# Kernel optimization log

Measured on AMD Instinct MI355X. Metric: run time of the kernel, lower is better.

The kernel has to match this reference:

```python
import jax, jax.numpy as jnp
import numpy as np

# dims (Nemotron-H 8B class mamba mixer)
HID = 4096      # hidden_size
NH = 128        # mamba_num_heads
HD = 64         # mamba_head_dim
DIN = NH * HD   # intermediate_size = 8192
G = 8           # n_groups
N = 128         # ssm_state_size
K = 4           # conv_kernel
CS = 256        # chunk_size
EPS = 1e-5
GROUP_SIZE = DIN // G
CONV_DIM = DIN + 2 * G * N           # 10240
PROJ = DIN + CONV_DIM + NH           # 18560 = gate | xBC | dt


def segment_sum(x):
    """x: [..., k] -> [..., k, k]; out[i,j] = sum_{m=j+1..i} x[m], -inf above diag."""
    k = x.shape[-1]
    xe = jnp.broadcast_to(x[..., None], x.shape + (k,))
    xe = jnp.where(jnp.tril(jnp.ones((k, k), bool), -1), xe, 0.0)
    s = jnp.cumsum(xe, axis=-2)
    return jnp.where(jnp.tril(jnp.ones((k, k), bool), 0), s, -jnp.inf)


def setup_inputs() -> dict:
    key = jax.random.key(0)
    ks = jax.random.split(key, 9)
    std = 0.02
    return {
        "hidden_states": jax.random.normal(ks[0], (2, 2048, HID), jnp.float32),
        "in_proj_w": jax.random.normal(ks[1], (PROJ, HID), jnp.float32) * std,
        "conv_w": jax.random.normal(ks[2], (CONV_DIM, 1, K), jnp.float32) * 0.1,
        "conv_b": jax.random.normal(ks[3], (CONV_DIM,), jnp.float32) * 0.01,
        "dt_bias": jax.random.uniform(ks[4], (NH,), jnp.float32, -4.0, -2.0),
        "A_log": jnp.log(jax.random.uniform(ks[5], (NH,), jnp.float32, 1.0, 16.0)),
        "D": jnp.ones((NH,), jnp.float32),
        "norm_w": jnp.ones((DIN,), jnp.float32),
        "out_proj_w": jax.random.normal(ks[8], (HID, DIN), jnp.float32) * std,
    }


def reference(hidden_states, in_proj_w, conv_w, conv_b, dt_bias, A_log, D, norm_w, out_proj_w):
    b, l, _ = hidden_states.shape
    zxbcdt = hidden_states @ in_proj_w.T                       # [b,l,PROJ]
    gate = zxbcdt[..., :DIN]
    xBC = zxbcdt[..., DIN:DIN + CONV_DIM]
    dt = zxbcdt[..., DIN + CONV_DIM:]                          # [b,l,NH]

    # causal depthwise conv1d + silu
    conv = jax.lax.conv_general_dilated(
        jnp.transpose(xBC, (0, 2, 1)), conv_w, (1,), [(K - 1, 0)],
        feature_group_count=CONV_DIM, dimension_numbers=("NCH", "OIH", "NCH"))
    xBC = jax.nn.silu(jnp.transpose(conv + conv_b[None, :, None], (0, 2, 1)))

    x = xBC[..., :DIN].reshape(b, l, NH, HD)
    B = xBC[..., DIN:DIN + G * N].reshape(b, l, G, N)
    C = xBC[..., DIN + G * N:].reshape(b, l, G, N)
    B = jnp.repeat(B, NH // G, axis=2)                         # [b,l,NH,N]
    C = jnp.repeat(C, NH // G, axis=2)

    A = -jnp.exp(A_log)                                        # [NH]
    dt = jax.nn.softplus(dt + dt_bias)                         # [b,l,NH]; limit (0,inf) is a no-op

    pad = (CS - l % CS) % CS
    def padl(t):
        return jnp.pad(t, [(0, 0), (0, pad)] + [(0, 0)] * (t.ndim - 2))

    D_res = D[None, None, :, None] * padl(x)                   # [b,L,NH,HD]
    xs = x * dt[..., None]
    Adt = A[None, None, :] * dt                                # [b,l,NH]

    nc = (l + pad) // CS
    def chunk(t):
        return padl(t).reshape((b, nc, CS) + t.shape[2:])
    xs, B, C = chunk(xs), chunk(B), chunk(C)                   # [b,c,k,h,*]
    Ac = jnp.transpose(chunk(Adt), (0, 3, 1, 2))               # [b,h,c,k]
    A_cumsum = jnp.cumsum(Ac, axis=-1)

    # 1. intra-chunk (diagonal blocks)
    L = jnp.exp(segment_sum(Ac))                               # [b,h,c,k,k]
    Gm = jnp.einsum("bcihn,bcjhn->bhcij", C, B)
    Y_diag = jnp.einsum("bhcij,bcjhd->bcihd", Gm * L, xs)

    # 2. chunk states
    decay_states = jnp.exp(A_cumsum[..., -1:] - A_cumsum)      # [b,h,c,k]
    states = jnp.einsum("bckhn,bhck,bckhd->bchdn", B, decay_states, xs)

    # 3. inter-chunk recurrence
    A_tail = jnp.pad(A_cumsum[..., -1], ((0, 0), (0, 0), (1, 0)))
    decay_chunk = jnp.exp(segment_sum(A_tail))                 # [b,h,c+1,c+1]
    states = jnp.concatenate([jnp.zeros_like(states[:, :1]), states], axis=1)
    new_states = jnp.einsum("bhzc,bchdn->bzhdn", decay_chunk, states)
    states = new_states[:, :-1]                                # [b,c,h,d,n]

    # 4. state -> output
    state_decay = jnp.exp(A_cumsum)                            # [b,h,c,k]
    Y_off = jnp.einsum("bckhn,bchdn,bhck->bckhd", C, states, state_decay)

    y = (Y_diag + Y_off).reshape(b, l + pad, NH, HD) + D_res
    y = y[:, :l].reshape(b, l, DIN)

    # gated grouped RMSNorm
    y = y * jax.nn.silu(gate)
    yg = y.reshape(b, l, G, GROUP_SIZE)
    var = jnp.mean(yg * yg, axis=-1, keepdims=True)
    y = (yg * jax.lax.rsqrt(var + EPS)).reshape(b, l, DIN) * norm_w
    return y @ out_proj_w.T
```

## Files before the change

### kernel.cpp

```cpp
#include <hip/hip_runtime.h>
#include <hip/hip_bf16.h>
#include <math.h>

#define HID 4096
#define NH 128
#define HD 64
#define DIN 8192
#define G 8
#define NSTATE 128
#define CS 256
#define GROUP_SIZE 1024
#define CONV_DIM 10240
#define ZXW 18432
#define BATCH 2
#define SEQ 2048
#define NT (BATCH*SEQ)
#define NC 8
#define DTSK 16

typedef __attribute__((ext_vector_type(8))) short bf16x8;
typedef __attribute__((ext_vector_type(4))) float f32x4;
typedef __attribute__((ext_vector_type(8))) unsigned short u16x8;
typedef __attribute__((ext_vector_type(4))) unsigned short u16x4;

__device__ __forceinline__ float sigmoidf_(float x){ return 1.f/(1.f+expf(-x)); }
__device__ __forceinline__ float siluf_(float x){ return x*sigmoidf_(x); }
__device__ __forceinline__ float softplusf_(float x){ return (x>20.f)? x : log1pf(expf(x)); }
__device__ __forceinline__ float b2f(unsigned short u){ union{unsigned int i; float f;} x; x.i = ((unsigned int)u)<<16; return x.f; }
__device__ __forceinline__ unsigned short f2b(float f){ __hip_bfloat16 h = __float2bfloat16(f); return *(unsigned short*)&h; }

__device__ __forceinline__ void gload_lds16(const void* g, void* l) {
  __builtin_amdgcn_global_load_lds((const __attribute__((address_space(1))) unsigned int*)g,
                                   (__attribute__((address_space(3))) unsigned int*)l, 16, 0, 0);
}
__device__ __forceinline__ bf16x8 ld8bf(const __hip_bfloat16* p){ return *(const bf16x8*)p; }

__device__ __forceinline__ void cast8(const float* in, __hip_bfloat16* out) {
  const float4* p = (const float4*)in;
  float4 a = p[0], b = p[1];
  union { __hip_bfloat16 h[8]; int4 v; } o;
  o.h[0]=__float2bfloat16(a.x); o.h[1]=__float2bfloat16(a.y);
  o.h[2]=__float2bfloat16(a.z); o.h[3]=__float2bfloat16(a.w);
  o.h[4]=__float2bfloat16(b.x); o.h[5]=__float2bfloat16(b.y);
  o.h[6]=__float2bfloat16(b.z); o.h[7]=__float2bfloat16(b.w);
  *(int4*)out = o.v;
}

__global__ __launch_bounds__(256)
void cast2_kernel(const float* __restrict__ w_in, __hip_bfloat16* __restrict__ w_in_bf,
                  const float* __restrict__ w_out, __hip_bfloat16* __restrict__ w_out_bf) {
  const size_t n1 = (size_t)ZXW*HID/8;
  const size_t n2 = (size_t)HID*DIN/8;
  const size_t ntot = n1 + n2;
  size_t i = (size_t)blockIdx.x * 256 + threadIdx.x;
  size_t stride = (size_t)gridDim.x * 256;
  for (; i < ntot; i += stride) {
    if (i < n1)  cast8(w_in + i*8,      w_in_bf + i*8);
    else         cast8(w_out+ (i-n1)*8, w_out_bf+ (i-n1)*8);
  }
}

template<bool OUT_BF16>
__global__ __launch_bounds__(512)
void gemm_bf16_256(const __hip_bfloat16* __restrict__ A, const __hip_bfloat16* __restrict__ B,
                   void* __restrict__ Cout, int M, int N, int K) {
  const int nMt = M >> 8, nNt = N >> 8;
  const int nwg = nMt * nNt;
  const int cpx = nwg >> 3;
  const int lin = blockIdx.x;
  const int swz = (lin & 7) * cpx + (lin >> 3);
  const int mt = swz % nMt, ntile = swz / nMt;
  const int rowBase = mt << 8;
  const int colBase = ntile << 8;

  __shared__ short As[4][8192];
  __shared__ short Bs[4][8192];

  const int tid = threadIdx.x;
  const int lane = tid & 63, wid = tid >> 6;
  const int wr = wid >> 2, wc = wid & 3;
  const int l15 = lane & 15, l4 = lane >> 4;

  const int r0 = tid >> 2,        c0 = (tid & 3) ^ ((r0 >> 1) & 3);
  const int r1 = (512+tid) >> 2,  c1 = ((512+tid) & 3) ^ ((r1 >> 1) & 3);
  const __hip_bfloat16* gA0 = A + (size_t)(rowBase + r0)*K + c0*8;
  const __hip_bfloat16* gA1 = A + (size_t)(rowBase + r1)*K + c1*8;
  const __hip_bfloat16* gB0 = B + (size_t)(colBase + r0)*K + c0*8;
  const __hip_bfloat16* gB1 = B + (size_t)(colBase + r1)*K + c1*8;
  const int ld0 = wid*512, ld1 = 4096 + wid*512;

#define STAGE_A(q, kt) do { \
    gload_lds16(gA0 + (size_t)(kt)*32, (void*)&As[q][ld0]); \
    gload_lds16(gA1 + (size_t)(kt)*32, (void*)&As[q][ld1]); \
  } while(0)
#define STAGE_B(q, kt) do { \
    gload_lds16(gB0 + (size_t)(kt)*32, (void*)&Bs[q][ld0]); \
    gload_lds16(gB1 + (size_t)(kt)*32, (void*)&Bs[q][ld1]); \
  } while(0)

  int aoff[8], boff[4];
  #pragma unroll
  for (int m=0;m<8;++m){ int r = wr*128 + m*16 + l15; aoff[m] = r*32 + ((l4 ^ ((r>>1)&3))*8); }
  #pragma unroll
  for (int n=0;n<4;++n){ int r = wc*64  + n*16 + l15; boff[n] = r*32 + ((l4 ^ ((r>>1)&3))*8); }

  f32x4 acc[8][4] = {};
  const int NKT = K >> 5;

  STAGE_A(0,0); STAGE_B(0,0);
  STAGE_A(1,1); STAGE_B(1,1);
  STAGE_A(2,2); STAGE_B(2,2);
  asm volatile("s_waitcnt vmcnt(8)" ::: "memory");
  __builtin_amdgcn_s_barrier();

  for (int t = 0; t < NKT; ++t) {
    const short* ab = &As[t&3][0];
    const short* bb = &Bs[t&3][0];
    const int q3 = (t+3)&3;
    bf16x8 a[4], b[4], a2[4];
    #pragma unroll
    for (int m=0;m<4;++m) a[m] = *(const bf16x8*)&ab[aoff[m]];
    #pragma unroll
    for (int n=0;n<4;++n) b[n] = *(const bf16x8*)&bb[boff[n]];
    if (t + 3 < NKT) STAGE_A(q3, t+3);
    __builtin_amdgcn_s_barrier();
    asm volatile("s_waitcnt lgkmcnt(0)" ::: "memory");
    __builtin_amdgcn_sched_barrier(0);
    __builtin_amdgcn_s_setprio(1);
    #pragma unroll
    for (int m=0;m<4;++m)
      #pragma unroll
      for (int n=0;n<4;++n)
        acc[m][n] = __builtin_amdgcn_mfma_f32_16x16x32_bf16(a[m], b[n], acc[m][n], 0, 0, 0);
    __builtin_amdgcn_s_setprio(0);
    __builtin_amdgcn_s_barrier();
    #pragma unroll
    for (int m=0;m<4;++m) a2[m] = *(const bf16x8*)&ab[aoff[m+4]];
    if (t + 3 < NKT) STAGE_B(q3, t+3);
    const int rem = NKT - 1 - t;
    if (rem >= 3)      asm volatile("s_waitcnt vmcnt(8)" ::: "memory");
    else if (rem == 2) asm volatile("s_waitcnt vmcnt(4)" ::: "memory");
    else if (rem == 1) asm volatile("s_waitcnt vmcnt(0)" ::: "memory");
    __builtin_amdgcn_s_barrier();
    asm volatile("s_waitcnt lgkmcnt(0)" ::: "memory");
    __builtin_amdgcn_sched_barrier(0);
    __builtin_amdgcn_s_setprio(1);
    #pragma unroll
    for (int m=0;m<4;++m)
      #pragma unroll
      for (int n=0;n<4;++n)
        acc[m+4][n] = __builtin_amdgcn_mfma_f32_16x16x32_bf16(a2[m], b[n], acc[m+4][n], 0, 0, 0);
    __builtin_amdgcn_s_setprio(0);
    __builtin_amdgcn_s_barrier();
  }
#undef STAGE_A
#undef STAGE_B

  #pragma unroll
  for (int m=0;m<8;++m) {
    int row0 = rowBase + wr*128 + m*16 + l4*4;
    #pragma unroll
    for (int n=0;n<4;++n) {
      int col = colBase + wc*64 + n*16 + l15;
      #pragma unroll
      for (int j=0;j<4;++j) {
        if (OUT_BF16)
          ((__hip_bfloat16*)Cout)[(size_t)(row0+j)*N + col] = __float2bfloat16(acc[m][n][j]);
        else
          ((float*)Cout)[(size_t)(row0+j)*N + col] = acc[m][n][j];
      }
    }
  }
}

__global__ __launch_bounds__(256)
void dt_gemm_splitk(const float* __restrict__ A, const float* __restrict__ B,
                    float* __restrict__ partial, __hip_bfloat16* __restrict__ hs_bf) {
  __shared__ float As[16][132];
  __shared__ float Bs[16][132];
  const int tid = threadIdx.x;
  const int tx = tid & 15, ty = tid >> 4;
  const int rowBase = blockIdx.y * 128;
  const int k0 = blockIdx.x * (HID/DTSK);
  float acc[8][8] = {};
  for (int kt = k0; kt < k0 + HID/DTSK; kt += 16) {
    for (int e = tid; e < 128*16; e += 256) {
      int r = e >> 4, c = e & 15;
      float av = A[(size_t)(rowBase + r) * HID + kt + c];
      As[c][r] = av;
      hs_bf[(size_t)(rowBase + r) * HID + kt + c] = __float2bfloat16(av);
      Bs[c][r] = B[(size_t)r * HID + kt + c];
    }
    __syncthreads();
    #pragma unroll
    for (int kk = 0; kk < 16; ++kk) {
      float a[8], bv[8];
      #pragma unroll
      for (int i = 0; i < 8; ++i) a[i] = As[kk][ty*8+i];
      #pragma unroll
      for (int j = 0; j < 8; ++j) bv[j] = Bs[kk][tx*8+j];
      #pragma unroll
      for (int i = 0; i < 8; ++i)
        #pragma unroll
        for (int j = 0; j < 8; ++j)
          acc[i][j] += a[i]*bv[j];
    }
    __syncthreads();
  }
  float* outp = partial + (size_t)blockIdx.x * NT * NH;
  for (int i = 0; i < 8; ++i) {
    size_t ro = (size_t)(rowBase + ty*8 + i) * NH + tx*8;
    #pragma unroll
    for (int j = 0; j < 8; ++j) outp[ro + j] = acc[i][j];
  }
}

__global__ __launch_bounds__(256)
void dt_scan_kernel(const float* __restrict__ partial, const float* __restrict__ dt_bias,
                    const float* __restrict__ A_log, float* __restrict__ dt_sp,
                    float* __restrict__ Acs) {
  int bid = blockIdx.x;
  int c = bid % NC;
  int h = (bid / NC) % NH;
  int b = bid / (NC*NH);
  int k = threadIdx.x;
  int t = b*SEQ + c*CS + k;
  float raw = dt_bias[h];
  #pragma unroll
  for (int sk = 0; sk < DTSK; ++sk) raw += partial[(size_t)sk*NT*NH + (size_t)t*NH + h];
  float dtv = softplusf_(raw);
  dt_sp[(size_t)t*NH + h] = dtv;
  float adt = -expf(A_log[h]) * dtv;
  __shared__ float s[CS];
  s[k] = adt;
  __syncthreads();
  for (int off = 1; off < CS; off <<= 1) {
    float v = (k >= off) ? s[k-off] : 0.f;
    __syncthreads();
    s[k] += v;
    __syncthreads();
  }
  Acs[((size_t)(b*NH + h)*NC + c)*CS + k] = s[k];
}

__global__ __launch_bounds__(256)
void conv_fused_kernel(const __hip_bfloat16* __restrict__ zx, const float* __restrict__ w,
                       const float* __restrict__ bias,
                       const float* __restrict__ dt_sp, const float* __restrict__ Acs,
                       __hip_bfloat16* __restrict__ xsT, __hip_bfloat16* __restrict__ xwT,
                       __hip_bfloat16* __restrict__ Bbf, __hip_bfloat16* __restrict__ Cbf,
                       __hip_bfloat16* __restrict__ BT) {
  const int tt = blockIdx.x;
  const int ct = blockIdx.y;
  const int t0 = tt*64;
  const int ch0 = ct*64;
  const int tid = threadIdx.x;
  __shared__ unsigned short T[64][72];
  __shared__ float dts[64], ews[64];

  const bool isX = (ch0 < DIN);
  const bool isB = (ch0 >= DIN) && (ch0 < DIN + G*NSTATE);

  if (isX && tid < 64) {
    int h = ch0 >> 6;
    int t = t0 + tid;
    dts[tid] = dt_sp[(size_t)t*NH + h];
    int b = t0 >> 11, cc = (t0 >> 8) & 7, k0 = t0 & 255;
    const float* acs = Acs + ((size_t)(b*NH+h)*NC + cc)*CS;
    ews[tid] = __expf(acs[CS-1] - acs[k0 + tid]);
  }

  const int l0 = t0 & (SEQ-1);
  #pragma unroll
  for (int it = 0; it < 2; ++it) {
    int r = tid >> 2;
    int c8 = (tid & 3) + it*4;
    int cb = ch0 + c8*8;
    float acc[8];
    *(float4*)&acc[0] = *(const float4*)&bias[cb];
    *(float4*)&acc[4] = *(const float4*)&bias[cb+4];
    float4 wv[8];
    #pragma unroll
    for (int q=0;q<8;++q) wv[q] = *(const float4*)&w[(cb+q)*4];
    #pragma unroll
    for (int k=0;k<4;++k) {
      if (l0 + r - 3 + k >= 0) {
        u16x8 v = *(const u16x8*)&zx[(size_t)(t0+r-3+k)*ZXW + DIN + cb];
        #pragma unroll
        for (int q=0;q<8;++q) acc[q] += b2f(v[q]) * ((const float*)&wv[q])[k];
      }
    }
    u16x8 o;
    #pragma unroll
    for (int q=0;q<8;++q) o[q] = f2b(siluf_(acc[q]));
    if (isX || isB) {
      #pragma unroll
      for (int q=0;q<8;++q) T[c8*8+q][r] = o[q];
    }
    if (!isX) {
      if (isB) *(u16x8*)&Bbf[(size_t)(t0+r)*(G*NSTATE) + (cb - DIN)] = o;
      else     *(u16x8*)&Cbf[(size_t)(t0+r)*(G*NSTATE) + (cb - DIN - G*NSTATE)] = o;
    }
  }
  if (!isX && !isB) return;
  __syncthreads();
  #pragma unroll
  for (int it = 0; it < 2; ++it) {
    int ch = tid >> 2;
    int tc = (tid & 3) + it*4;
    u16x8 v = *(const u16x8*)&T[ch][tc*8];
    if (isX) {
      u16x8 a, wv2;
      #pragma unroll
      for (int q=0;q<8;++q) {
        float f = b2f(v[q]);
        float fs = f * dts[tc*8+q];
        a[q]   = f2b(fs);
        wv2[q] = f2b(fs * ews[tc*8+q]);
      }
      *(u16x8*)&xsT[(size_t)(ch0+ch)*NT + t0 + tc*8] = a;
      *(u16x8*)&xwT[(size_t)(ch0+ch)*NT + t0 + tc*8] = wv2;
    } else {
      *(u16x8*)&BT[(size_t)(ch0 - DIN + ch)*NT + t0 + tc*8] = v;
    }
  }
}

__global__ __launch_bounds__(256)
void chunk_states_fused(const __hip_bfloat16* __restrict__ xwT, const __hip_bfloat16* __restrict__ BT,
                        const float* __restrict__ Acs, __hip_bfloat16* __restrict__ states_bf) {
  int h = blockIdx.x, b = blockIdx.y;
  int g = h >> 4;
  int tid = threadIdx.x, lane = tid & 63, w = tid >> 6;
  int l15 = lane & 15, l4 = lane >> 4;
  int n0 = w*32;
  f32x4 S[4][2] = {};
  for (int c = 0; c < NC; ++c) {
    int tbase = b*SEQ + c*CS;
    const __hip_bfloat16* xp = xwT + (size_t)(h*64 + l15)*NT + tbase + l4*8;
    const __hip_bfloat16* bp = BT + (size_t)(g*128 + n0 + l15)*NT + tbase + l4*8;
    f32x4 acc[4][2] = {};
    for (int kc = 0; kc < 8; ++kc) {
      bf16x8 xf[4], bf2[2];
      #pragma unroll
      for (int tm=0;tm<4;++tm) xf[tm] = ld8bf(xp + (size_t)(tm*16)*NT + kc*32);
      #pragma unroll
      for (int tn=0;tn<2;++tn) bf2[tn] = ld8bf(bp + (size_t)(tn*16)*NT + kc*32);
      #pragma unroll
      for (int tm=0;tm<4;++tm)
        #pragma unroll
        for (int tn=0;tn<2;++tn)
          acc[tm][tn] = __builtin_amdgcn_mfma_f32_16x16x32_bf16(xf[tm], bf2[tn], acc[tm][tn], 0, 0, 0);
    }
    __hip_bfloat16* out = states_bf + ((size_t)(b*NC + c)*NH + h)*(HD*NSTATE);
    float decay = expf(Acs[((size_t)(b*NH+h)*NC + c)*CS + CS-1]);
    #pragma unroll
    for (int tm=0;tm<4;++tm)
      #pragma unroll
      for (int tn=0;tn<2;++tn)
        #pragma unroll
        for (int q=0;q<4;++q) {
          out[(size_t)(tm*16 + l4*4 + q)*NSTATE + n0 + tn*16 + l15] = __float2bfloat16(S[tm][tn][q]);
          S[tm][tn][q] = S[tm][tn][q]*decay + acc[tm][tn][q];
        }
  }
}

__global__ __launch_bounds__(256)
void y_mfma_kernel(const __hip_bfloat16* __restrict__ zx,
                   const __hip_bfloat16* __restrict__ Cn,
                   const __hip_bfloat16* __restrict__ Bn,
                   const __hip_bfloat16* __restrict__ xsT,
                   const __hip_bfloat16* __restrict__ Sbf,
                   const float* __restrict__ dt_sp,
                   const float* __restrict__ Acs,
                   const float* __restrict__ Dp,
                   __hip_bfloat16* __restrict__ ybf) {
  int h = blockIdx.x;
  int bc = blockIdx.y;
  int c = bc & 7, b = bc >> 3;
  int g = h >> 4;
  int tbase = b*SEQ + c*CS;
  int tid = threadIdx.x, lane = tid & 63, w = tid >> 6;
  int l15 = lane & 15, l4 = lane >> 4;
  int i0 = w*64;
  __shared__ float acs_s[CS];
  __shared__ unsigned short P[4][64][72];
  acs_s[tid] = Acs[((size_t)(b*NH+h)*NC + c)*CS + tid];
  __syncthreads();

  float acs_i[4], rd[4];
  float Dh = Dp[h];
  #pragma unroll
  for (int ti=0;ti<4;++ti) {
    int ig = i0 + ti*16 + l15;
    acs_i[ti] = acs_s[ig];
    rd[ti] = Dh / dt_sp[(size_t)(tbase+ig)*NH + h];
  }
  const __hip_bfloat16* Cbase = Cn + (size_t)tbase*1024 + g*128;
  const __hip_bfloat16* Bbase = Bn + (size_t)tbase*1024 + g*128;
  const __hip_bfloat16* xbase = xsT + (size_t)(h*64 + l15)*NT + tbase;

  f32x4 accY[4][4] = {};
  for (int jb = 0; jb <= w; ++jb) {
    int j0 = jb*64;
    f32x4 sacc[4][4] = {};
    for (int kc = 0; kc < 4; ++kc) {
      bf16x8 bfr[4], cfr[4];
      #pragma unroll
      for (int tj=0;tj<4;++tj) bfr[tj] = ld8bf(Bbase + (size_t)(j0 + tj*16 + l15)*1024 + kc*32 + l4*8);
      #pragma unroll
      for (int ti=0;ti<4;++ti) cfr[ti] = ld8bf(Cbase + (size_t)(i0 + ti*16 + l15)*1024 + kc*32 + l4*8);
      #pragma unroll
      for (int tj=0;tj<4;++tj)
        #pragma unroll
        for (int ti=0;ti<4;++ti)
          sacc[tj][ti] = __builtin_amdgcn_mfma_f32_16x16x32_bf16(bfr[tj], cfr[ti], sacc[tj][ti], 0, 0, 0);
    }
    #pragma unroll
    for (int tj=0;tj<4;++tj)
      #pragma unroll
      for (int ti=0;ti<4;++ti) {
        int ig = i0 + ti*16 + l15;
        float ai = acs_i[ti];
        u16x4 pk;
        #pragma unroll
        for (int q=0;q<4;++q) {
          int jg = j0 + tj*16 + l4*4 + q;
          float v = (jg <= ig) ? sacc[tj][ti][q] * __expf(ai - acs_s[jg]) : 0.f;
          if (jg == ig) v += rd[ti];
          pk[q] = f2b(v);
        }
        *(u16x4*)&P[w][ti*16 + l15][tj*16 + l4*4] = pk;
      }
    #pragma unroll
    for (int kc2 = 0; kc2 < 2; ++kc2) {
      bf16x8 xf[4], pf[4];
      #pragma unroll
      for (int tm=0;tm<4;++tm) xf[tm] = ld8bf(xbase + (size_t)(tm*16)*NT + j0 + kc2*32 + l4*8);
      #pragma unroll
      for (int ti=0;ti<4;++ti) pf[ti] = *(const bf16x8*)&P[w][ti*16 + l15][kc2*32 + l4*8];
      #pragma unroll
      for (int tm=0;tm<4;++tm)
        #pragma unroll
        for (int ti=0;ti<4;++ti)
          accY[tm][ti] = __builtin_amdgcn_mfma_f32_16x16x32_bf16(xf[tm], pf[ti], accY[tm][ti], 0, 0, 0);
    }
  }
  const __hip_bfloat16* Sb = Sbf + ((size_t)bc*NH + h)*(HD*NSTATE);
  f32x4 oacc[4][4] = {};
  for (int kc = 0; kc < 4; ++kc) {
    bf16x8 sf[4], cfr[4];
    #pragma unroll
    for (int tm=0;tm<4;++tm) sf[tm] = ld8bf(Sb + (size_t)(tm*16 + l15)*NSTATE + kc*32 + l4*8);
    #pragma unroll
    for (int ti=0;ti<4;++ti) cfr[ti] = ld8bf(Cbase + (size_t)(i0 + ti*16 + l15)*1024 + kc*32 + l4*8);
    #pragma unroll
    for (int tm=0;tm<4;++tm)
      #pragma unroll
      for (int ti=0;ti<4;++ti)
        oacc[tm][ti] = __builtin_amdgcn_mfma_f32_16x16x32_bf16(sf[tm], cfr[ti], oacc[tm][ti], 0, 0, 0);
  }
  #pragma unroll
  for (int ti=0;ti<4;++ti) {
    int ig = i0 + ti*16 + l15;
    int t = tbase + ig;
    float sd = __expf(acs_i[ti]);
    #pragma unroll
    for (int tm=0;tm<4;++tm) {
      int ch0 = h*64 + tm*16 + l4*4;
      u16x4 gv = *(const u16x4*)&zx[(size_t)t*ZXW + ch0];
      u16x4 out;
      #pragma unroll
      for (int q=0;q<4;++q) {
        float yv = accY[tm][ti][q] + sd * oacc[tm][ti][q];
        yv *= siluf_(b2f(gv[q]));
        out[q] = f2b(yv);
      }
      *(u16x4*)&ybf[(size_t)t*DIN + ch0] = out;
    }
  }
}

__global__ __launch_bounds__(256)
void groupnorm_bf16_kernel(unsigned short* __restrict__ y, const float* __restrict__ norm_w) {
  int bid = blockIdx.x;
  int g = bid % G;
  int t = bid / G;
  unsigned short* yp = y + (size_t)t*DIN + g*GROUP_SIZE;
  int tid = threadIdx.x;
  u16x4 v = *(const u16x4*)&yp[tid*4];
  float f[4]; float ss = 0.f;
  #pragma unroll
  for (int j=0;j<4;++j) { f[j] = b2f(v[j]); ss += f[j]*f[j]; }
  #pragma unroll
  for (int off = 32; off > 0; off >>= 1) ss += __shfl_xor(ss, off);
  __shared__ float wsum[4];
  int wave = tid >> 6;
  if ((tid & 63) == 0) wsum[wave] = ss;
  __syncthreads();
  float tot = wsum[0]+wsum[1]+wsum[2]+wsum[3];
  float rs = rsqrtf(tot/(float)GROUP_SIZE + 1e-5f);
  const float* nw = norm_w + g*GROUP_SIZE + tid*4;
  u16x4 o;
  #pragma unroll
  for (int j=0;j<4;++j) o[j] = f2b(f[j] * rs * nw[j]);
  *(u16x4*)&yp[tid*4] = o;
}

extern "C" void kernel_launch(void* const* d_in, const int* in_sizes, int n_in,
                              void* d_out, int out_size, void* d_ws, size_t ws_size,
                              hipStream_t stream) {
  const float* hs        = (const float*)d_in[0];
  const float* in_proj_w = (const float*)d_in[1];
  const float* conv_w    = (const float*)d_in[2];
  const float* conv_b    = (const float*)d_in[3];
  const float* dt_bias   = (const float*)d_in[4];
  const float* A_log     = (const float*)d_in[5];
  const float* Dp        = (const float*)d_in[6];
  const float* norm_w    = (const float*)d_in[7];
  const float* out_proj_w= (const float*)d_in[8];
  float* outp = (float*)d_out;

  char* ws = (char*)d_ws;
  __hip_bfloat16* zx_bf = (__hip_bfloat16*)ws;
  char* p = ws + (size_t)NT*ZXW*2;
  __hip_bfloat16* B_bf  = (__hip_bfloat16*)p; p += (size_t)NT*G*NSTATE*2;
  __hip_bfloat16* C_bf  = (__hip_bfloat16*)p; p += (size_t)NT*G*NSTATE*2;
  __hip_bfloat16* BT    = (__hip_bfloat16*)p; p += (size_t)NT*G*NSTATE*2;
  __hip_bfloat16* y_bf  = (__hip_bfloat16*)p; p += (size_t)NT*DIN*2;
  float* dtb    = (float*)p;  p += (size_t)NT*NH*4;
  float* Acs    = (float*)p;  p += (size_t)BATCH*NH*NC*CS*4;
  float* dt_part = (float*)y_bf;
  char* F = p;
  __hip_bfloat16* w_in_bf   = (__hip_bfloat16*)F;
  __hip_bfloat16* xsT       = (__hip_bfloat16*)F;
  __hip_bfloat16* xwT       = (__hip_bfloat16*)(F + 67108864);
  __hip_bfloat16* hs_bf     = (__hip_bfloat16*)(F + 150994944);
  __hip_bfloat16* states_bf = (__hip_bfloat16*)(F + 150994944);
  char* F2 = F + 150994944 + 33554432;
  __hip_bfloat16* w_out_bf  = (__hip_bfloat16*)F2;

  dt_gemm_splitk<<<dim3(DTSK, NT/128), 256, 0, stream>>>(hs, in_proj_w + (size_t)ZXW*HID, dt_part, hs_bf);
  dt_scan_kernel<<<BATCH*NH*NC, CS, 0, stream>>>(dt_part, dt_bias, A_log, dtb, Acs);

  cast2_kernel<<<4096, 256, 0, stream>>>(in_proj_w, w_in_bf, out_proj_w, w_out_bf);

  gemm_bf16_256<true><<<dim3((NT/256)*(ZXW/256)), 512, 0, stream>>>(
      hs_bf, w_in_bf, zx_bf, NT, ZXW, HID);

  conv_fused_kernel<<<dim3(NT/64, CONV_DIM/64), 256, 0, stream>>>(
      zx_bf, conv_w, conv_b, dtb, Acs, xsT, xwT, B_bf, C_bf, BT);

  chunk_states_fused<<<dim3(NH, BATCH), 256, 0, stream>>>(xwT, BT, Acs, states_bf);

  y_mfma_kernel<<<dim3(NH, BATCH*NC), 256, 0, stream>>>(zx_bf, C_bf, B_bf, xsT, states_bf, dtb, Acs, Dp, y_bf);
  groupnorm_bf16_kernel<<<NT*G, 256, 0, stream>>>((unsigned short*)y_bf, norm_w);

  gemm_bf16_256<false><<<dim3((NT/256)*(HID/256)), 512, 0, stream>>>(
      y_bf, w_out_bf, outp, NT, HID, DIN);
}
```

Measured before the change: 1.798 ms.

## Restructure bf16 GEMM mainloop into 8-phase ping-pong pipeline with K=64 tiles

```diff
diff --git a/kernel.cpp b/kernel.cpp
--- a/kernel.cpp
+++ b/kernel.cpp
@@ -61,7 +61,7 @@
 }
 
 template<bool OUT_BF16>
-__global__ __launch_bounds__(512)
+__global__ __launch_bounds__(512, 2)
 void gemm_bf16_256(const __hip_bfloat16* __restrict__ A, const __hip_bfloat16* __restrict__ B,
                    void* __restrict__ Cout, int M, int N, int K) {
   const int nMt = M >> 8, nNt = N >> 8;
@@ -73,88 +73,105 @@
   const int rowBase = mt << 8;
   const int colBase = ntile << 8;
 
-  __shared__ short As[4][8192];
-  __shared__ short Bs[4][8192];
+  __shared__ short As[2][2][8192];
+  __shared__ short Bs[2][2][8192];
 
   const int tid = threadIdx.x;
   const int lane = tid & 63, wid = tid >> 6;
   const int wr = wid >> 2, wc = wid & 3;
   const int l15 = lane & 15, l4 = lane >> 4;
 
-  const int r0 = tid >> 2,        c0 = (tid & 3) ^ ((r0 >> 1) & 3);
-  const int r1 = (512+tid) >> 2,  c1 = ((512+tid) & 3) ^ ((r1 >> 1) & 3);
-  const __hip_bfloat16* gA0 = A + (size_t)(rowBase + r0)*K + c0*8;
-  const __hip_bfloat16* gA1 = A + (size_t)(rowBase + r1)*K + c1*8;
-  const __hip_bfloat16* gB0 = B + (size_t)(colBase + r0)*K + c0*8;
-  const __hip_bfloat16* gB1 = B + (size_t)(colBase + r1)*K + c1*8;
-  const int ld0 = wid*512, ld1 = 4096 + wid*512;
-
-#define STAGE_A(q, kt) do { \
-    gload_lds16(gA0 + (size_t)(kt)*32, (void*)&As[q][ld0]); \
-    gload_lds16(gA1 + (size_t)(kt)*32, (void*)&As[q][ld1]); \
+  const int r0 = tid >> 2;
+  const int c0 = (tid & 3) ^ ((r0 >> 1) & 3);
+  const __hip_bfloat16* gA = A + (size_t)(rowBase + r0)*K + c0*8;
+  const __hip_bfloat16* gB = B + (size_t)(colBase + r0)*K + c0*8;
+  const int wdst = wid * 512;
+
+#define STG(Ld, gp, h, kt) do { \
+    gload_lds16(gp + (size_t)((h)*128)*K + (size_t)(kt)*64,      (void*)&(Ld)[wdst]); \
+    gload_lds16(gp + (size_t)((h)*128)*K + (size_t)(kt)*64 + 32, (void*)&(Ld)[4096 + wdst]); \
   } while(0)
-#define STAGE_B(q, kt) do { \
-    gload_lds16(gB0 + (size_t)(kt)*32, (void*)&Bs[q][ld0]); \
-    gload_lds16(gB1 + (size_t)(kt)*32, (void*)&Bs[q][ld1]); \
+
+  const int xg = (l4 ^ ((l15 >> 1) & 3)) * 8;
+  int aofs[8], bofs[4];
+  #pragma unroll
+  for (int m=0;m<8;++m) aofs[m] = (m*16 + l15)*32 + xg;
+  #pragma unroll
+  for (int n=0;n<4;++n) bofs[n] = ((wc&1)*64 + n*16 + l15)*32 + xg;
+
+  bf16x8 Af[4][2], Bf[4][2];
+  f32x4 acc[8][4] = {};
+
+#define RDA(bb, mh) do { \
+    const short* s_ = &As[bb][wr][0]; \
+    _Pragma("unroll") for (int m=0;m<4;++m) { \
+      Af[m][0] = *(const bf16x8*)&s_[aofs[(mh)*4+m]]; \
+      Af[m][1] = *(const bf16x8*)&s_[4096 + aofs[(mh)*4+m]]; } \
   } while(0)
-
-  int aoff[8], boff[4];
-  #pragma unroll
-  for (int m=0;m<8;++m){ int r = wr*128 + m*16 + l15; aoff[m] = r*32 + ((l4 ^ ((r>>1)&3))*8); }
-  #pragma unroll
-  for (int n=0;n<4;++n){ int r = wc*64  + n*16 + l15; boff[n] = r*32 + ((l4 ^ ((r>>1)&3))*8); }
-
-  f32x4 acc[8][4] = {};
-  const int NKT = K >> 5;
-
-  STAGE_A(0,0); STAGE_B(0,0);
-  STAGE_A(1,1); STAGE_B(1,1);
-  STAGE_A(2,2); STAGE_B(2,2);
-  asm volatile("s_waitcnt vmcnt(8)" ::: "memory");
+#define RDB(bb, nh) do { \
+    const short* s_ = &Bs[bb][wc>>1][0]; \
+    _Pragma("unroll") for (int n=0;n<2;++n) { \
+      Bf[(nh)*2+n][0] = *(const bf16x8*)&s_[bofs[(nh)*2+n]]; \
+      Bf[(nh)*2+n][1] = *(const bf16x8*)&s_[4096 + bofs[(nh)*2+n]]; } \
+  } while(0)
+#define MFQ(mh, nh) do { \
+    __builtin_amdgcn_s_setprio(1); \
+    _Pragma("unroll") for (int m=0;m<4;++m) \
+      _Pragma("unroll") for (int n=0;n<2;++n) \
+        _Pragma("unroll") for (int ks=0;ks<2;++ks) \
+          acc[(mh)*4+m][(nh)*2+n] = __builtin_amdgcn_mfma_f32_16x16x32_bf16( \
+              Af[m][ks], Bf[(nh)*2+n][ks], acc[(mh)*4+m][(nh)*2+n], 0, 0, 0); \
+    __builtin_amdgcn_s_setprio(0); \
+  } while(0)
+#define FENCE() do { \
+    __builtin_amdgcn_s_barrier(); \
+    asm volatile("s_waitcnt lgkmcnt(0)" ::: "memory"); \
+    __builtin_amdgcn_sched_barrier(0); \
+  } while(0)
+#define ENDP() __builtin_amdgcn_s_barrier()
+
+  const int NKT = K >> 6;
+  const int NU = NKT >> 1;
+
+  STG(Bs[0][0], gB, 0, 0); STG(As[0][0], gA, 0, 0);
+  STG(Bs[0][1], gB, 1, 0); STG(As[0][1], gA, 1, 0);
+  STG(Bs[1][0], gB, 0, 1); STG(As[1][0], gA, 0, 1);
+  asm volatile("s_waitcnt vmcnt(4)" ::: "memory");
   __builtin_amdgcn_s_barrier();
 
-  for (int t = 0; t < NKT; ++t) {
-    const short* ab = &As[t&3][0];
-    const short* bb = &Bs[t&3][0];
-    const int q3 = (t+3)&3;
-    bf16x8 a[4], b[4], a2[4];
-    #pragma unroll
-    for (int m=0;m<4;++m) a[m] = *(const bf16x8*)&ab[aoff[m]];
-    #pragma unroll
-    for (int n=0;n<4;++n) b[n] = *(const bf16x8*)&bb[boff[n]];
-    if (t + 3 < NKT) STAGE_A(q3, t+3);
-    __builtin_amdgcn_s_barrier();
-    asm volatile("s_waitcnt lgkmcnt(0)" ::: "memory");
-    __builtin_amdgcn_sched_barrier(0);
-    __builtin_amdgcn_s_setprio(1);
-    #pragma unroll
-    for (int m=0;m<4;++m)
-      #pragma unroll
-      for (int n=0;n<4;++n)
-        acc[m][n] = __builtin_amdgcn_mfma_f32_16x16x32_bf16(a[m], b[n], acc[m][n], 0, 0, 0);
-    __builtin_amdgcn_s_setprio(0);
-    __builtin_amdgcn_s_barrier();
-    #pragma unroll
-    for (int m=0;m<4;++m) a2[m] = *(const bf16x8*)&ab[aoff[m+4]];
-    if (t + 3 < NKT) STAGE_B(q3, t+3);
-    const int rem = NKT - 1 - t;
-    if (rem >= 3)      asm volatile("s_waitcnt vmcnt(8)" ::: "memory");
-    else if (rem == 2) asm volatile("s_waitcnt vmcnt(4)" ::: "memory");
-    else if (rem == 1) asm volatile("s_waitcnt vmcnt(0)" ::: "memory");
-    __builtin_amdgcn_s_barrier();
-    asm volatile("s_waitcnt lgkmcnt(0)" ::: "memory");
-    __builtin_amdgcn_sched_barrier(0);
-    __builtin_amdgcn_s_setprio(1);
-    #pragma unroll
-    for (int m=0;m<4;++m)
-      #pragma unroll
-      for (int n=0;n<4;++n)
-        acc[m+4][n] = __builtin_amdgcn_mfma_f32_16x16x32_bf16(a2[m], b[n], acc[m+4][n], 0, 0, 0);
-    __builtin_amdgcn_s_setprio(0);
-    __builtin_amdgcn_s_barrier();
-  }
-#undef STAGE_A
-#undef STAGE_B
+  for (int u = 0; u < NU; ++u) {
+    const int T = 2*u;
+    const bool last = (u == NU-1);
+    RDA(0, 0); RDB(0, 0);
+    STG(Bs[1][1], gB, 1, T+1);
+    FENCE(); MFQ(0, 0); ENDP();
+    RDB(0, 1);
+    STG(As[1][1], gA, 1, T+1);
+    FENCE(); MFQ(0, 1); ENDP();
+    RDA(0, 1);
+    if (!last) STG(Bs[0][0], gB, 0, T+2);
+    FENCE(); MFQ(1, 1); ENDP();
+    if (!last) STG(As[0][0], gA, 0, T+2);
+    FENCE(); MFQ(1, 0); ENDP();
+    RDA(1, 0); RDB(1, 0);
+    if (!last) { STG(Bs[0][1], gB, 1, T+2); asm volatile("s_waitcnt vmcnt(6)" ::: "memory"); }
+    else       { asm volatile("s_waitcnt vmcnt(0)" ::: "memory"); }
+    FENCE(); MFQ(0, 0); ENDP();
+    RDB(1, 1);
+    if (!last) STG(As[0][1], gA, 1, T+2);
+    FENCE(); MFQ(0, 1); ENDP();
+    RDA(1, 1);
+    if (!last) STG(Bs[1][0], gB, 0, T+3);
+    FENCE(); MFQ(1, 1); ENDP();
+    if (!last) { STG(As[1][0], gA, 0, T+3); asm volatile("s_waitcnt vmcnt(4)" ::: "memory"); }
+    FENCE(); MFQ(1, 0); ENDP();
+  }
+#undef STG
+#undef RDA
+#undef RDB
+#undef MFQ
+#undef FENCE
+#undef ENDP
 
   #pragma unroll
   for (int m=0;m<8;++m) {
```

New measurement: 1.783 ms. Within noise of the previous version (-0.9%).
